# Kernel tuning notes

Hardware: AMD Instinct MI355X
Metric: run time of the kernel (lower is better)

## Reference

```python
import jax, jax.numpy as jnp
import numpy as np

C_IN = 1024
C_INTER = 512
EPS = 1e-5
STD = 0.01


def _conv1x1(x, w, b):
    # x: [B,C,H,W], w: [O,C] (1x1 conv kernel squeezed), b: [O]
    return jnp.einsum('bchw,oc->bohw', x, w) + b[None, :, None, None]


def setup_inputs() -> dict:
    key = jax.random.key(0)
    ks = jax.random.split(key, 12)
    def w(k, o, i):
        return jax.random.normal(k, (o, i), jnp.float32) * STD
    def b(k, o):
        return jax.random.normal(k, (o,), jnp.float32) * STD
    return {
        'x': jax.random.normal(ks[0], (8, C_IN, 64, 64), jnp.float32),
        'theta_w': w(ks[1], C_INTER, C_IN), 'theta_b': b(ks[2], C_INTER),
        'phi_w': w(ks[3], C_INTER, C_IN), 'phi_b': b(ks[4], C_INTER),
        'g_w': w(ks[5], C_INTER, C_IN), 'g_b': b(ks[6], C_INTER),
        'wz_w': w(ks[7], C_IN, C_INTER), 'wz_b': b(ks[8], C_IN),
        'bn_gamma': jax.random.normal(ks[9], (C_IN,), jnp.float32) * 0.1,
        'bn_beta': jax.random.normal(ks[10], (C_IN,), jnp.float32) * 0.1,
    }


def reference(x, theta_w, theta_b, phi_w, phi_b, g_w, g_b, wz_w, wz_b, bn_gamma, bn_beta):
    B, C, H, W = x.shape
    # theta on full-res input: [B, Ci, H*W]
    theta = _conv1x1(x, theta_w, theta_b).reshape(B, C_INTER, H * W)
    # 2x2 stride-2 max pool for phi/g path
    xp = jax.lax.reduce_window(x, -jnp.inf, jax.lax.max,
                               (1, 1, 2, 2), (1, 1, 2, 2), 'VALID')
    Hp, Wp = xp.shape[2], xp.shape[3]
    phi = _conv1x1(xp, phi_w, phi_b).reshape(B, C_INTER, Hp * Wp)
    g = _conv1x1(xp, g_w, g_b).reshape(B, C_INTER, Hp * Wp)
    # attention: [B, H*W, Hp*Wp], scaled softmax
    attn = jnp.einsum('bcn,bcm->bnm', theta, phi) * (C_INTER ** -0.5)
    attn = jax.nn.softmax(attn, axis=-1)
    # aggregate: [B, Ci, H*W]
    y = jnp.einsum('bcm,bnm->bcn', g, attn).reshape(B, C_INTER, H, W)
    z = _conv1x1(y, wz_w, wz_b)
    # BatchNorm2d (training-mode batch stats, biased var)
    mean = z.mean(axis=(0, 2, 3), keepdims=True)
    var = jnp.mean((z - mean) ** 2, axis=(0, 2, 3), keepdims=True)
    z = (z - mean) * jax.lax.rsqrt(var + EPS)
    z = z * bn_gamma[None, :, None, None] + bn_beta[None, :, None, None]
    return x + z
```

## Files before the change

### kernel.cpp

```cpp
#include <hip/hip_runtime.h>

typedef unsigned short u16;
typedef unsigned int u32;
typedef __attribute__((ext_vector_type(8))) short bf16x8;
typedef __attribute__((ext_vector_type(4))) float f32x4;

__device__ __forceinline__ u16 f2bf(float f) {
  u32 u = __builtin_bit_cast(u32, f);
  u = u + 0x7FFFu + ((u >> 16) & 1u);
  return (u16)(u >> 16);
}
__device__ __forceinline__ float bf2f(u16 s) {
  return __builtin_bit_cast(float, (u32)s << 16);
}

__device__ __forceinline__ void gload_lds16(const u16* g, u16* l) {
  __builtin_amdgcn_global_load_lds(
      (const __attribute__((address_space(1))) u32*)g,
      (__attribute__((address_space(3))) u32*)l, 16, 0, 0);
}

__global__ __launch_bounds__(256) void k_cvt(const float* __restrict__ s,
                                             u16* __restrict__ d) {
  int i = (blockIdx.x * 256 + threadIdx.x) * 4;
  float4 v = *(const float4*)(s + i);
  u32 lo = (u32)f2bf(v.x) | ((u32)f2bf(v.y) << 16);
  u32 hi = (u32)f2bf(v.z) | ((u32)f2bf(v.w) << 16);
  uint2 o; o.x = lo; o.y = hi;
  *(uint2*)(d + i) = o;
}

__global__ __launch_bounds__(256) void k_transpose_pool(
    const float* __restrict__ x, u16* __restrict__ xT, u16* __restrict__ xpT) {
  __shared__ u16 lds[32][520];
  const int t = threadIdx.x;
  const int c0 = blockIdx.x * 32;
  const int h0 = blockIdx.y * 8;
  const int b = blockIdx.z;
  const float* xb = x + ((size_t)b * 1024 + c0) * 4096 + h0 * 64;
  for (int ci = 0; ci < 32; ++ci) {
    float2 v = *(const float2*)(xb + (size_t)ci * 4096 + t * 2);
    lds[ci][t * 2] = f2bf(v.x);
    lds[ci][t * 2 + 1] = f2bf(v.y);
  }
  __syncthreads();
  {
    const int nsub = t >> 5, ci = t & 31;
    size_t base = ((size_t)b * 4096 + h0 * 64) * 1024 + c0 + ci;
    for (int ng = 0; ng < 64; ++ng) {
      int n = ng * 8 + nsub;
      xT[base + (size_t)n * 1024] = lds[ci][n];
    }
  }
  {
    const int msub = t >> 5, ci = t & 31;
    size_t base = ((size_t)b * 1024 + (h0 >> 1) * 32) * 1024 + c0 + ci;
    for (int mg = 0; mg < 16; ++mg) {
      int ml = mg * 8 + msub;
      int mhl = ml >> 5, mw = ml & 31;
      int n0 = mhl * 128 + mw * 2;
      float v = fmaxf(fmaxf(bf2f(lds[ci][n0]), bf2f(lds[ci][n0 + 1])),
                      fmaxf(bf2f(lds[ci][n0 + 64]), bf2f(lds[ci][n0 + 65])));
      xpT[base + (size_t)(mhl * 32 + mw) * 1024] = f2bf(v);
    }
  }
}

template <int BIAS_MODE>
__global__ __launch_bounds__(256, 2) void gemm_nt(
    const u16* __restrict__ A, long aBS, const u16* __restrict__ Bm, long bBS,
    u16* __restrict__ Cm, long cBS, const float* __restrict__ bias, int N,
    int K, float scale) {
  __shared__ u16 Alds[128 * 32];
  __shared__ u16 Blds[128 * 32];
  const int t = threadIdx.x;
  const int b = blockIdx.z;
  const int bm = blockIdx.y, bn = blockIdx.x;
  const u16* Ab = A + (size_t)b * aBS + (size_t)bm * 128 * K;
  const u16* Bb = Bm + (size_t)b * bBS + (size_t)bn * 128 * K;

  const int lane = t & 63;
  const int w = t >> 6;
  const int wrow = w >> 1, wcol = w & 1;
  const int lr = lane & 15;
  const int kg = lane >> 4;

  f32x4 acc[4][4] = {};

  const int e0 = t * 8;
  const int r0 = e0 >> 5;
  const int k0i = e0 & 31;
  const int steps = K >> 5;
  for (int ks = 0; ks < steps; ++ks) {
    const int kb = ks * 32;
    gload_lds16(Ab + (size_t)r0 * K + kb + k0i, &Alds[e0]);
    gload_lds16(Ab + (size_t)(r0 + 64) * K + kb + k0i, &Alds[e0 + 2048]);
    gload_lds16(Bb + (size_t)r0 * K + kb + k0i, &Blds[e0]);
    gload_lds16(Bb + (size_t)(r0 + 64) * K + kb + k0i, &Blds[e0 + 2048]);
    __syncthreads();
    bf16x8 af[4], bfr[4];
#pragma unroll
    for (int i = 0; i < 4; ++i) {
      af[i] = *(const bf16x8*)&Alds[(wrow * 64 + i * 16 + lr) * 32 + kg * 8];
      bfr[i] = *(const bf16x8*)&Blds[(wcol * 64 + i * 16 + lr) * 32 + kg * 8];
    }
#pragma unroll
    for (int i = 0; i < 4; ++i)
#pragma unroll
      for (int j = 0; j < 4; ++j)
        acc[i][j] = __builtin_amdgcn_mfma_f32_16x16x32_bf16(af[i], bfr[j],
                                                            acc[i][j], 0, 0, 0);
    __syncthreads();
  }
  u16* Cb = Cm + (size_t)b * cBS;
#pragma unroll
  for (int i = 0; i < 4; ++i) {
#pragma unroll
    for (int j = 0; j < 4; ++j) {
      int row0 = bm * 128 + wrow * 64 + i * 16 + kg * 4;
      int col = bn * 128 + wcol * 64 + j * 16 + lr;
      float bj = (BIAS_MODE == 2) ? bias[col] : 0.f;
#pragma unroll
      for (int r = 0; r < 4; ++r) {
        float v = acc[i][j][r] * scale;
        if (BIAS_MODE == 1) v += bias[row0 + r];
        if (BIAS_MODE == 2) v += bj;
        Cb[(size_t)(row0 + r) * N + col] = f2bf(v);
      }
    }
  }
}

__global__ __launch_bounds__(256) void k_softmax(u16* __restrict__ S) {
  const int t = threadIdx.x;
  const int lane = t & 63;
  const size_t row = (size_t)blockIdx.x * 4 + (t >> 6);
  u16* p = S + row * 1024 + lane * 16;
  uint4 d0 = *(const uint4*)p;
  uint4 d1 = *(const uint4*)(p + 8);
  u32 u[8] = {d0.x, d0.y, d0.z, d0.w, d1.x, d1.y, d1.z, d1.w};
  float v[16];
#pragma unroll
  for (int i = 0; i < 8; ++i) {
    v[2 * i] = bf2f((u16)(u[i] & 0xffff));
    v[2 * i + 1] = bf2f((u16)(u[i] >> 16));
  }
  float m = v[0];
#pragma unroll
  for (int i = 1; i < 16; ++i) m = fmaxf(m, v[i]);
  for (int o = 32; o > 0; o >>= 1) m = fmaxf(m, __shfl_xor(m, o));
  const float LOG2E = 1.44269504088896f;
  float s = 0.f;
#pragma unroll
  for (int i = 0; i < 16; ++i) {
    v[i] = exp2f((v[i] - m) * LOG2E);
    s += v[i];
  }
  for (int o = 32; o > 0; o >>= 1) s += __shfl_xor(s, o);
  float inv = 1.0f / s;
#pragma unroll
  for (int i = 0; i < 8; ++i)
    u[i] = (u32)f2bf(v[2 * i] * inv) | ((u32)f2bf(v[2 * i + 1] * inv) << 16);
  uint4 o0; o0.x = u[0]; o0.y = u[1]; o0.z = u[2]; o0.w = u[3];
  uint4 o1; o1.x = u[4]; o1.y = u[5]; o1.z = u[6]; o1.w = u[7];
  *(uint4*)p = o0;
  *(uint4*)(p + 8) = o1;
}

__global__ __launch_bounds__(256) void k_stats(const u16* __restrict__ z,
                                               float2* __restrict__ stats) {
  const int o = blockIdx.x;
  const int t = threadIdx.x;
  float s = 0.f, q = 0.f;
  for (int b = 0; b < 8; ++b) {
    const u16* p = z + ((size_t)b * 1024 + o) * 4096;
    for (int i = t * 4; i < 4096; i += 1024) {
      uint2 d = *(const uint2*)(p + i);
      float a0 = bf2f((u16)(d.x & 0xffff)), a1 = bf2f((u16)(d.x >> 16));
      float a2 = bf2f((u16)(d.y & 0xffff)), a3 = bf2f((u16)(d.y >> 16));
      s += a0 + a1 + a2 + a3;
      q += a0 * a0 + a1 * a1 + a2 * a2 + a3 * a3;
    }
  }
  for (int o2 = 32; o2 > 0; o2 >>= 1) {
    s += __shfl_xor(s, o2);
    q += __shfl_xor(q, o2);
  }
  __shared__ float2 red[4];
  if ((t & 63) == 0) red[t >> 6] = make_float2(s, q);
  __syncthreads();
  if (t == 0) {
    float S_ = 0.f, Q_ = 0.f;
    for (int i = 0; i < 4; ++i) { S_ += red[i].x; Q_ += red[i].y; }
    stats[o] = make_float2(S_, Q_);
  }
}

__global__ __launch_bounds__(256) void k_apply(
    const float* __restrict__ x, const u16* __restrict__ z,
    const float2* __restrict__ stats, const float* __restrict__ gamma,
    const float* __restrict__ beta, float* __restrict__ out) {
  size_t i4 = (size_t)blockIdx.x * 256 + threadIdx.x;
  size_t e = i4 * 4;
  int c = (int)((e >> 12) & 1023);
  float2 st = stats[c];
  const float cnt = 1.0f / 32768.0f;
  float mean = st.x * cnt;
  float var = st.y * cnt - mean * mean;
  float g = rsqrtf(var + 1e-5f) * gamma[c];
  float sh = beta[c] - mean * g;
  float4 xv = *(const float4*)(x + e);
  uint2 zd = *(const uint2*)(z + e);
  float z0 = bf2f((u16)(zd.x & 0xffff)), z1 = bf2f((u16)(zd.x >> 16));
  float z2 = bf2f((u16)(zd.y & 0xffff)), z3 = bf2f((u16)(zd.y >> 16));
  float4 ov;
  ov.x = xv.x + z0 * g + sh;
  ov.y = xv.y + z1 * g + sh;
  ov.z = xv.z + z2 * g + sh;
  ov.w = xv.w + z3 * g + sh;
  *(float4*)(out + e) = ov;
}

extern "C" void kernel_launch(void* const* d_in, const int* in_sizes, int n_in,
                              void* d_out, int out_size, void* d_ws,
                              size_t ws_size, hipStream_t stream) {
  const float* x = (const float*)d_in[0];
  const float* theta_w = (const float*)d_in[1];
  const float* theta_b = (const float*)d_in[2];
  const float* phi_w = (const float*)d_in[3];
  const float* phi_b = (const float*)d_in[4];
  const float* g_w = (const float*)d_in[5];
  const float* g_b = (const float*)d_in[6];
  const float* wz_w = (const float*)d_in[7];
  const float* wz_b = (const float*)d_in[8];
  const float* gamma = (const float*)d_in[9];
  const float* beta = (const float*)d_in[10];
  float* out = (float*)d_out;

  char* w = (char*)d_ws;
  const size_t MiB = (size_t)1 << 20;
  u16* WT = (u16*)(w + 0 * MiB);
  u16* WP = (u16*)(w + 1 * MiB);
  u16* WG = (u16*)(w + 2 * MiB);
  u16* WZ = (u16*)(w + 3 * MiB);
  u16* XT = (u16*)(w + 4 * MiB);
  u16* XPT = (u16*)(w + 68 * MiB);
  u16* THETA = (u16*)(w + 84 * MiB);
  u16* PHI = (u16*)(w + 116 * MiB);
  u16* G = (u16*)(w + 124 * MiB);
  u16* S = XT;
  u16* YT = (u16*)(w + 132 * MiB);
  u16* Z = S;
  float2* stats = (float2*)(w + 164 * MiB);

  k_cvt<<<512, 256, 0, stream>>>(theta_w, WT);
  k_cvt<<<512, 256, 0, stream>>>(phi_w, WP);
  k_cvt<<<512, 256, 0, stream>>>(g_w, WG);
  k_cvt<<<512, 256, 0, stream>>>(wz_w, WZ);
  k_transpose_pool<<<dim3(32, 8, 8), 256, 0, stream>>>(x, XT, XPT);
  gemm_nt<2><<<dim3(4, 32, 8), 256, 0, stream>>>(
      XT, (long)4096 * 1024, WT, 0, THETA, (long)4096 * 512, theta_b, 512,
      1024, 1.0f);
  gemm_nt<2><<<dim3(4, 8, 8), 256, 0, stream>>>(
      XPT, (long)1024 * 1024, WP, 0, PHI, (long)1024 * 512, phi_b, 512, 1024,
      1.0f);
  gemm_nt<1><<<dim3(8, 4, 8), 256, 0, stream>>>(
      WG, 0, XPT, (long)1024 * 1024, G, (long)512 * 1024, g_b, 1024, 1024,
      1.0f);
  gemm_nt<0><<<dim3(8, 32, 8), 256, 0, stream>>>(
      THETA, (long)4096 * 512, PHI, (long)1024 * 512, S, (long)4096 * 1024,
      nullptr, 1024, 512, 0.04419417382415922f);
  k_softmax<<<8192, 256, 0, stream>>>(S);
  gemm_nt<0><<<dim3(4, 32, 8), 256, 0, stream>>>(
      S, (long)4096 * 1024, G, (long)512 * 1024, YT, (long)4096 * 512, nullptr,
      512, 1024, 1.0f);
  gemm_nt<1><<<dim3(32, 8, 8), 256, 0, stream>>>(
      WZ, 0, YT, (long)4096 * 512, Z, (long)1024 * 4096, wz_b, 4096, 512,
      1.0f);
  k_stats<<<1024, 256, 0, stream>>>(Z, stats);
  k_apply<<<32768, 256, 0, stream>>>(x, Z, stats, gamma, beta, out);

  (void)in_sizes; (void)n_in; (void)out_size; (void)ws_size;
}
```

Before: 598.1 us.

## Vectorize transpose-pool stores with swizzled LDS and double-buffer GEMM LDS tiles

The transpose/pool kernel now loads float4 inputs and stages a 128x64 tile in LDS with an XOR swizzle. It then writes 16-byte bf16x8 rows to xT and xpT instead of scattered 2-byte strided stores, and the pooled max is computed on vectors. The intent is to remove the heavily uncoalesced scalar global writes in the transpose pass. Separately, the NT GEMM gets two LDS buffers per operand and prefetches the next K-slice right after the barrier, which drops one barrier per iteration and overlaps global-to-LDS loads with MFMA work. The cost is double the GEMM's LDS use, which may reduce occupancy.

```diff
diff --git a/kernel.cpp b/kernel.cpp
--- a/kernel.cpp
+++ b/kernel.cpp
@@ -32,37 +32,56 @@
 
 __global__ __launch_bounds__(256) void k_transpose_pool(
     const float* __restrict__ x, u16* __restrict__ xT, u16* __restrict__ xpT) {
-  __shared__ u16 lds[32][520];
+  __shared__ u16 lds[128 * 64];
   const int t = threadIdx.x;
-  const int c0 = blockIdx.x * 32;
-  const int h0 = blockIdx.y * 8;
+  const int c0 = blockIdx.x * 64;
+  const int by = blockIdx.y;
   const int b = blockIdx.z;
-  const float* xb = x + ((size_t)b * 1024 + c0) * 4096 + h0 * 64;
-  for (int ci = 0; ci < 32; ++ci) {
-    float2 v = *(const float2*)(xb + (size_t)ci * 4096 + t * 2);
-    lds[ci][t * 2] = f2bf(v.x);
-    lds[ci][t * 2 + 1] = f2bf(v.y);
+
+  {
+    const int nf = (t & 31) * 4;
+    const int swz = 8 * (t & 7);
+    const float* xb =
+        x + ((size_t)(b * 1024 + c0 + (t >> 5)) * 4096) + by * 128 + nf;
+#pragma unroll
+    for (int u = 0; u < 8; ++u) {
+      const int c_l = (t >> 5) + 8 * u;
+      float4 v = *(const float4*)(xb + (size_t)(8 * u) * 4096);
+      const int col = c_l ^ swz;
+      lds[(nf + 0) * 64 + col] = f2bf(v.x);
+      lds[(nf + 1) * 64 + col] = f2bf(v.y);
+      lds[(nf + 2) * 64 + col] = f2bf(v.z);
+      lds[(nf + 3) * 64 + col] = f2bf(v.w);
+    }
   }
   __syncthreads();
   {
-    const int nsub = t >> 5, ci = t & 31;
-    size_t base = ((size_t)b * 4096 + h0 * 64) * 1024 + c0 + ci;
-    for (int ng = 0; ng < 64; ++ng) {
-      int n = ng * 8 + nsub;
-      xT[base + (size_t)n * 1024] = lds[ci][n];
+#pragma unroll
+    for (int v = 0; v < 4; ++v) {
+      const int idx = t + 256 * v;
+      const int n_l = idx >> 3;
+      const int cb = (idx & 7) * 8;
+      const int col = cb ^ (8 * ((n_l >> 2) & 7));
+      bf16x8 d = *(const bf16x8*)&lds[n_l * 64 + col];
+      *(bf16x8*)&xT[((size_t)b * 4096 + by * 128 + n_l) * 1024 + c0 + cb] = d;
     }
   }
   {
-    const int msub = t >> 5, ci = t & 31;
-    size_t base = ((size_t)b * 1024 + (h0 >> 1) * 32) * 1024 + c0 + ci;
-    for (int mg = 0; mg < 16; ++mg) {
-      int ml = mg * 8 + msub;
-      int mhl = ml >> 5, mw = ml & 31;
-      int n0 = mhl * 128 + mw * 2;
-      float v = fmaxf(fmaxf(bf2f(lds[ci][n0]), bf2f(lds[ci][n0 + 1])),
-                      fmaxf(bf2f(lds[ci][n0 + 64]), bf2f(lds[ci][n0 + 65])));
-      xpT[base + (size_t)(mhl * 32 + mw) * 1024] = f2bf(v);
-    }
+    const int m_w = t >> 3;
+    const int cb = (t & 7) * 8;
+    const int na = 2 * m_w, nb = na + 1, nc = na + 64, nd = na + 65;
+    bf16x8 va = *(const bf16x8*)&lds[na * 64 + (cb ^ (8 * ((na >> 2) & 7)))];
+    bf16x8 vb = *(const bf16x8*)&lds[nb * 64 + (cb ^ (8 * ((nb >> 2) & 7)))];
+    bf16x8 vc = *(const bf16x8*)&lds[nc * 64 + (cb ^ (8 * ((nc >> 2) & 7)))];
+    bf16x8 vd = *(const bf16x8*)&lds[nd * 64 + (cb ^ (8 * ((nd >> 2) & 7)))];
+    bf16x8 o;
+#pragma unroll
+    for (int j = 0; j < 8; ++j) {
+      float m = fmaxf(fmaxf(bf2f((u16)va[j]), bf2f((u16)vb[j])),
+                      fmaxf(bf2f((u16)vc[j]), bf2f((u16)vd[j])));
+      o[j] = (short)f2bf(m);
+    }
+    *(bf16x8*)&xpT[((size_t)b * 1024 + by * 32 + m_w) * 1024 + c0 + cb] = o;
   }
 }
 
@@ -71,8 +90,8 @@
     const u16* __restrict__ A, long aBS, const u16* __restrict__ Bm, long bBS,
     u16* __restrict__ Cm, long cBS, const float* __restrict__ bias, int N,
     int K, float scale) {
-  __shared__ u16 Alds[128 * 32];
-  __shared__ u16 Blds[128 * 32];
+  __shared__ u16 Alds[2][128 * 32];
+  __shared__ u16 Blds[2][128 * 32];
   const int t = threadIdx.x;
   const int b = blockIdx.z;
   const int bm = blockIdx.y, bn = blockIdx.x;
@@ -91,18 +110,30 @@
   const int r0 = e0 >> 5;
   const int k0i = e0 & 31;
   const int steps = K >> 5;
+
+#define STAGE(buf, ks)                                                   \
+  do {                                                                   \
+    const int kb = (ks) * 32;                                            \
+    gload_lds16(Ab + (size_t)r0 * K + kb + k0i, &Alds[buf][e0]);         \
+    gload_lds16(Ab + (size_t)(r0 + 64) * K + kb + k0i,                   \
+                &Alds[buf][e0 + 2048]);                                  \
+    gload_lds16(Bb + (size_t)r0 * K + kb + k0i, &Blds[buf][e0]);         \
+    gload_lds16(Bb + (size_t)(r0 + 64) * K + kb + k0i,                   \
+                &Blds[buf][e0 + 2048]);                                  \
+  } while (0)
+
+  STAGE(0, 0);
   for (int ks = 0; ks < steps; ++ks) {
-    const int kb = ks * 32;
-    gload_lds16(Ab + (size_t)r0 * K + kb + k0i, &Alds[e0]);
-    gload_lds16(Ab + (size_t)(r0 + 64) * K + kb + k0i, &Alds[e0 + 2048]);
-    gload_lds16(Bb + (size_t)r0 * K + kb + k0i, &Blds[e0]);
-    gload_lds16(Bb + (size_t)(r0 + 64) * K + kb + k0i, &Blds[e0 + 2048]);
+    const int cur = ks & 1;
     __syncthreads();
+    if (ks + 1 < steps) STAGE(cur ^ 1, ks + 1);
     bf16x8 af[4], bfr[4];
 #pragma unroll
     for (int i = 0; i < 4; ++i) {
-      af[i] = *(const bf16x8*)&Alds[(wrow * 64 + i * 16 + lr) * 32 + kg * 8];
-      bfr[i] = *(const bf16x8*)&Blds[(wcol * 64 + i * 16 + lr) * 32 + kg * 8];
+      af[i] =
+          *(const bf16x8*)&Alds[cur][(wrow * 64 + i * 16 + lr) * 32 + kg * 8];
+      bfr[i] =
+          *(const bf16x8*)&Blds[cur][(wcol * 64 + i * 16 + lr) * 32 + kg * 8];
     }
 #pragma unroll
     for (int i = 0; i < 4; ++i)
@@ -110,8 +141,9 @@
       for (int j = 0; j < 4; ++j)
         acc[i][j] = __builtin_amdgcn_mfma_f32_16x16x32_bf16(af[i], bfr[j],
                                                             acc[i][j], 0, 0, 0);
-    __syncthreads();
-  }
+  }
+#undef STAGE
+
   u16* Cb = Cm + (size_t)b * cBS;
 #pragma unroll
   for (int i = 0; i < 4; ++i) {
@@ -257,7 +289,7 @@
   k_cvt<<<512, 256, 0, stream>>>(phi_w, WP);
   k_cvt<<<512, 256, 0, stream>>>(g_w, WG);
   k_cvt<<<512, 256, 0, stream>>>(wz_w, WZ);
-  k_transpose_pool<<<dim3(32, 8, 8), 256, 0, stream>>>(x, XT, XPT);
+  k_transpose_pool<<<dim3(16, 32, 8), 256, 0, stream>>>(x, XT, XPT);
   gemm_nt<2><<<dim3(4, 32, 8), 256, 0, stream>>>(
       XT, (long)4096 * 1024, WT, 0, THETA, (long)4096 * 512, theta_b, 512,
       1024, 1.0f);
```

Result: faster. 579.5 us (-3.1%).
